# Optimization experiments

Measured on AMD Instinct MI355X. Metric: run time of the kernel, lower is better.

## Reference

```python
import jax, jax.numpy as jnp
import numpy as np

D_MODEL = 1024
FF_SIZE = 4096
H = 16
DK = D_MODEL // H
MASK_VAL = -1e15
EPS = 1e-5


def setup_inputs() -> dict:
    key = jax.random.key(0)
    ks = jax.random.split(key, 16)
    B, M, d = 2, 2048, D_MODEL
    s = 1.0 / np.sqrt(d)
    inp = {
        "x": jax.random.normal(ks[0], (B, M, d), dtype=jnp.float32),
        "mask": jnp.ones((B, M), dtype=bool),
        "Wq": jax.random.normal(ks[1], (d, d), dtype=jnp.float32) * s,
        "bq": jnp.zeros((d,), jnp.float32),
        "Wk": jax.random.normal(ks[2], (d, d), dtype=jnp.float32) * s,
        "bk": jnp.zeros((d,), jnp.float32),
        "Wv": jax.random.normal(ks[3], (d, d), dtype=jnp.float32) * s,
        "bv": jnp.zeros((d,), jnp.float32),
        "W1": jax.random.normal(ks[4], (d, FF_SIZE), dtype=jnp.float32) * s,
        "b1": jnp.zeros((FF_SIZE,), jnp.float32),
        "W2": jax.random.normal(ks[5], (FF_SIZE, d), dtype=jnp.float32) / np.sqrt(FF_SIZE),
        "b2": jnp.zeros((d,), jnp.float32),
        "g1": jnp.ones((d,), jnp.float32),
        "beta1": jnp.zeros((d,), jnp.float32),
        "g2": jnp.ones((d,), jnp.float32),
        "beta2": jnp.zeros((d,), jnp.float32),
    }
    return inp


def _layernorm(x, g, b):
    mu = jnp.mean(x, axis=-1, keepdims=True)
    var = jnp.var(x, axis=-1, keepdims=True)
    return (x - mu) * jax.lax.rsqrt(var + EPS) * g + b


def _forward(x, mask, Wq, bq, Wk, bk, Wv, bv, W1, b1, W2, b2, g1, beta1, g2, beta2):
    B, M, d = x.shape
    q = (x @ Wq + bq).reshape(B, M, H, DK)
    k = (x @ Wk + bk).reshape(B, M, H, DK)
    v = (x @ Wv + bv).reshape(B, M, H, DK)
    # att: [B, H, Mq, Mk]
    att = jnp.einsum("bqhd,bkhd->bhqk", q, k)
    if mask is not None:
        m = (mask[:, None, :] & mask[:, :, None])[:, None, :, :]  # [B,1,Mq,Mk]
        att = jnp.where(m, att, MASK_VAL)
    # NOTE: original divides by d_model (not sqrt(dk))
    att = jax.nn.softmax(att / D_MODEL, axis=-1)
    attn_out = jnp.einsum("bhqk,bkhd->bqhd", att, v).reshape(B, M, d)
    h1 = _layernorm(x + attn_out, g1, beta1)
    ff = jax.nn.relu(h1 @ W1 + b1) @ W2 + b2
    return _layernorm(h1 + ff, g2, beta2)


def reference(x, mask, Wq, bq, Wk, bk, Wv, bv, W1, b1, W2, b2, g1, beta1, g2, beta2):
    return _forward(x, mask, Wq, bq, Wk, bk, Wv, bv, W1, b1, W2, b2, g1, beta1, g2, beta2)
```

## Files before the change

### kernel.cpp

```cpp
#include <hip/hip_runtime.h>
#include <hip/hip_bf16.h>


typedef __bf16 bf16;
typedef __attribute__((ext_vector_type(8))) __bf16 bf16x8;
typedef __attribute__((ext_vector_type(4))) __bf16 bf16x4;
typedef __attribute__((ext_vector_type(4))) float f32x4;

#define MFMA16(a, b, c) __builtin_amdgcn_mfma_f32_16x16x32_bf16(a, b, c, 0, 0, 0)

__device__ __forceinline__ void ld_g2l16(void* lds, const void* g) {
  __builtin_amdgcn_global_load_lds((const __attribute__((address_space(1))) void*)g,
                                   (__attribute__((address_space(3))) void*)lds,
                                   16, 0, 0);
}

__global__ __launch_bounds__(256) void detect_dtype(const void* __restrict__ x,
                                                    int* __restrict__ flag) {
  const unsigned short* u = (const unsigned short*)x;
  int cnt = 0;
  for (int i = threadIdx.x; i < 4096; i += 256) {
    const int e = (u[i] >> 7) & 0xFF;
    if (e >= 140) ++cnt;
  }
  __shared__ int sh[256];
  sh[threadIdx.x] = cnt;
  __syncthreads();
  for (int s = 128; s > 0; s >>= 1) {
    if (threadIdx.x < s) sh[threadIdx.x] += sh[threadIdx.x + s];
    __syncthreads();
  }
  if (threadIdx.x == 0) *flag = (sh[0] > 100) ? 1 : 0;
}

__device__ __forceinline__ bf16 load_any(const void* p, size_t i, int fl) {
  return fl ? (bf16)((const float*)p)[i] : ((const bf16*)p)[i];
}

__global__ __launch_bounds__(256) void convert_x(const void* __restrict__ in,
                                                 bf16* __restrict__ o,
                                                 const int* __restrict__ flag) {
  const int fl = *flag;
  const size_t i0 = (size_t)(blockIdx.x * 256 + threadIdx.x) * 4;
#pragma unroll
  for (int i = 0; i < 4; ++i) o[i0 + i] = load_any(in, i0 + i, fl);
}

__global__ __launch_bounds__(256) void convert_small(
    const void* p0, const void* p1, const void* p2, const void* p3,
    const void* p4, const void* p5, const void* p6, const void* p7,
    const void* p8, bf16* __restrict__ dst, const int* __restrict__ flag) {
  const int fl = *flag;
  const int t = blockIdx.x * 256 + threadIdx.x;
  const void* ps[9] = {p0, p1, p2, p3, p4, p5, p6, p7, p8};
  const int sz[9]  = {1024, 1024, 1024, 4096, 1024, 1024, 1024, 1024, 1024};
  const int off[9] = {0, 1024, 2048, 3072, 7168, 8192, 9216, 10240, 11264};
#pragma unroll
  for (int a = 0; a < 9; ++a)
    if (t < sz[a]) dst[off[a] + t] = load_any(ps[a], t, fl);
}

__global__ __launch_bounds__(256) void transpose_w(const void* __restrict__ in,
                                                   bf16* __restrict__ out,
                                                   int R, int C,
                                                   const int* __restrict__ flag) {
  const int fl = *flag;
  __shared__ bf16 t[32][33];
  const int r0 = blockIdx.y * 32, c0 = blockIdx.x * 32;
  const int tx = threadIdx.x, ty = threadIdx.y;
#pragma unroll
  for (int i = ty; i < 32; i += 8)
    t[i][tx] = load_any(in, (size_t)(r0 + i) * C + c0 + tx, fl);
  __syncthreads();
#pragma unroll
  for (int i = ty; i < 32; i += 8)
    out[(size_t)(c0 + i) * R + r0 + tx] = t[tx][i];
}

__global__ __launch_bounds__(256) void transpose_w3(const void* __restrict__ q,
                                                    const void* __restrict__ k,
                                                    const void* __restrict__ v,
                                                    bf16* __restrict__ out,
                                                    const int* __restrict__ flag) {
  const int fl = *flag;
  const int z = blockIdx.z;
  const void* in = (z == 0) ? q : (z == 1) ? k : v;
  bf16* o = out + (size_t)z * 1024 * 1024;
  __shared__ bf16 t[32][33];
  const int r0 = blockIdx.y * 32, c0 = blockIdx.x * 32;
  const int tx = threadIdx.x, ty = threadIdx.y;
#pragma unroll
  for (int i = ty; i < 32; i += 8)
    t[i][tx] = load_any(in, (size_t)(r0 + i) * 1024 + c0 + tx, fl);
  __syncthreads();
#pragma unroll
  for (int i = ty; i < 32; i += 8)
    o[(size_t)(c0 + i) * 1024 + r0 + tx] = t[tx][i];
}

__global__ __launch_bounds__(256) void transpose_v(const bf16* __restrict__ qkvb,
                                                   bf16* __restrict__ vT) {
  __shared__ bf16 t[32][33];
  const int bh = blockIdx.z;
  const int b = bh >> 4, h = bh & 15;
  const int m0 = blockIdx.x * 32, d0 = blockIdx.y * 32;
  const int tx = threadIdx.x, ty = threadIdx.y;
#pragma unroll
  for (int i = ty; i < 32; i += 8)
    t[i][tx] = qkvb[(size_t)(b * 2048 + m0 + i) * 3072 + 2048 + h * 64 + d0 + tx];
  __syncthreads();
#pragma unroll
  for (int i = ty; i < 32; i += 8)
    vT[((size_t)bh * 64 + d0 + i) * 2048 + m0 + tx] = t[tx][i];
}

__global__ __launch_bounds__(256) void gemm_bt(const bf16* __restrict__ A,
                                               const bf16* __restrict__ BT,
                                               const bf16* __restrict__ bias,
                                               bf16* __restrict__ C,
                                               int M, int N, int K, int relu) {
  __shared__ bf16 sA[2][128 * 32];
  __shared__ bf16 sB[2][128 * 32];
  const int tid = threadIdx.x;
  const int wave = tid >> 6, lane = tid & 63;
  const int wm = wave >> 1, wn = wave & 1;
  const int gx = N >> 7;
  const int L = blockIdx.x;
  const int x8 = L & 7;
  const int t1 = L >> 3;
  const int cb = t1 % gx;
  const int rb = (t1 / gx) * 8 + x8;
  const int bm = rb * 128, bn = cb * 128;
  const int m16 = lane & 15, kg = lane >> 4;
  const int srow = lane >> 2;
  const int sswz = ((lane & 3) ^ ((srow >> 1) & 3)) * 8;
  const int kswz = (kg ^ ((m16 >> 1) & 3)) * 8;

  f32x4 acc[4][4];
#pragma unroll
  for (int i = 0; i < 4; ++i)
#pragma unroll
    for (int j = 0; j < 4; ++j) acc[i][j] = (f32x4){0.f, 0.f, 0.f, 0.f};

  for (int k0 = 0; k0 < K; k0 += 64) {
#pragma unroll
    for (int i = 0; i < 2; ++i) {
      const int c = wave * 2 + i;
      const int row = c * 16 + srow;
#pragma unroll
      for (int h = 0; h < 2; ++h) {
        ld_g2l16(&sA[h][c * 512], A + (size_t)(bm + row) * K + k0 + h * 32 + sswz);
        ld_g2l16(&sB[h][c * 512], BT + (size_t)(bn + row) * K + k0 + h * 32 + sswz);
      }
    }
    __syncthreads();

#pragma unroll
    for (int ks = 0; ks < 2; ++ks) {
      bf16x8 af[4], bfr[4];
#pragma unroll
      for (int t = 0; t < 4; ++t) {
        af[t]  = *(const bf16x8*)&sA[ks][(wm * 64 + t * 16 + m16) * 32 + kswz];
        bfr[t] = *(const bf16x8*)&sB[ks][(wn * 64 + t * 16 + m16) * 32 + kswz];
      }
#pragma unroll
      for (int mt = 0; mt < 4; ++mt)
#pragma unroll
        for (int nt = 0; nt < 4; ++nt)
          acc[mt][nt] = MFMA16(af[mt], bfr[nt], acc[mt][nt]);
    }
    __syncthreads();
  }

  const int r0 = bm + wm * 64, c0 = bn + wn * 64;
#pragma unroll
  for (int nt = 0; nt < 4; ++nt) {
    const int col = c0 + nt * 16 + m16;
    const float bv = (float)bias[col];
#pragma unroll
    for (int mt = 0; mt < 4; ++mt) {
#pragma unroll
      for (int r = 0; r < 4; ++r) {
        const int row = r0 + mt * 16 + kg * 4 + r;
        float v = acc[mt][nt][r] + bv;
        if (relu) v = fmaxf(v, 0.f);
        C[(size_t)row * N + col] = (bf16)v;
      }
    }
  }
}

__global__ __launch_bounds__(256) void gemm_bt64_sk(const bf16* __restrict__ A,
                                                    const bf16* __restrict__ BT,
                                                    bf16* __restrict__ C0,
                                                    bf16* __restrict__ C1,
                                                    int M, int N, int Kf, int Kp) {
  __shared__ bf16 sA[2][128 * 32];
  __shared__ bf16 sB[2][64 * 32];
  const int tid = threadIdx.x;
  const int wave = tid >> 6, lane = tid & 63;
  const int L = blockIdx.x;
  const int x8 = L & 7;
  const int t1 = L >> 3;
  const int cb = t1 & 15;
  const int u = t1 >> 4;
  const int z = u & 1;
  const int rb = (u >> 1) * 8 + x8;
  const int bm = rb * 128, bn = cb * 64;
  const int kbase = z * Kp;
  const int m16 = lane & 15, kg = lane >> 4;
  const int srow = lane >> 2;
  const int sswz = ((lane & 3) ^ ((srow >> 1) & 3)) * 8;
  const int kswz = (kg ^ ((m16 >> 1) & 3)) * 8;

  f32x4 acc[2][4];
#pragma unroll
  for (int i = 0; i < 2; ++i)
#pragma unroll
    for (int j = 0; j < 4; ++j) acc[i][j] = (f32x4){0.f, 0.f, 0.f, 0.f};

  for (int k0 = 0; k0 < Kp; k0 += 64) {
#pragma unroll
    for (int i = 0; i < 2; ++i) {
      const int c = wave * 2 + i;
      const int row = bm + c * 16 + srow;
#pragma unroll
      for (int h = 0; h < 2; ++h)
        ld_g2l16(&sA[h][c * 512], A + (size_t)row * Kf + kbase + k0 + h * 32 + sswz);
    }
    {
      const int row = bn + wave * 16 + srow;
#pragma unroll
      for (int h = 0; h < 2; ++h)
        ld_g2l16(&sB[h][wave * 512], BT + (size_t)row * Kf + kbase + k0 + h * 32 + sswz);
    }
    __syncthreads();

#pragma unroll
    for (int ks = 0; ks < 2; ++ks) {
      bf16x8 af[2], bfr[4];
#pragma unroll
      for (int t = 0; t < 2; ++t)
        af[t] = *(const bf16x8*)&sA[ks][(wave * 32 + t * 16 + m16) * 32 + kswz];
#pragma unroll
      for (int t = 0; t < 4; ++t)
        bfr[t] = *(const bf16x8*)&sB[ks][(t * 16 + m16) * 32 + kswz];
#pragma unroll
      for (int mt = 0; mt < 2; ++mt)
#pragma unroll
        for (int nt = 0; nt < 4; ++nt)
          acc[mt][nt] = MFMA16(af[mt], bfr[nt], acc[mt][nt]);
    }
    __syncthreads();
  }

  bf16* C = z ? C1 : C0;
  const int r0 = bm + wave * 32;
#pragma unroll
  for (int nt = 0; nt < 4; ++nt) {
    const int col = bn + nt * 16 + m16;
#pragma unroll
    for (int mt = 0; mt < 2; ++mt) {
#pragma unroll
      for (int r = 0; r < 4; ++r) {
        const int row = r0 + mt * 16 + kg * 4 + r;
        C[(size_t)row * N + col] = (bf16)acc[mt][nt][r];
      }
    }
  }
}

__global__ __launch_bounds__(256) void attn_kernel(const bf16* __restrict__ qkvb,
                                                   const bf16* __restrict__ vT,
                                                   bf16* __restrict__ op0,
                                                   bf16* __restrict__ op1,
                                                   float* __restrict__ den0,
                                                   float* __restrict__ den1) {
  __shared__ bf16 sK[2][64 * 32];
  __shared__ bf16 sV[2][64 * 32];
  __shared__ bf16 pl[4][2][16 * 72];
  const int L = blockIdx.x;
  const int x8 = L & 7;
  const int t1 = L >> 3;
  const int qt = t1 & 15;
  const int c  = (t1 >> 4) * 8 + x8;
  const int h  = c & 15;
  const int z  = c >> 4;
  const int b = z >> 1, kh = z & 1;
  const int tid = threadIdx.x, wv = tid >> 6, lane = tid & 63;
  const int m16 = lane & 15, kg = lane >> 4;
  const int srow = lane >> 2;
  const int sswz = ((lane & 3) ^ ((srow >> 1) & 3)) * 8;
  const int kswz = (kg ^ ((m16 >> 1) & 3)) * 8;

  const float qs = 1.4426950408889634f / 1024.0f;
  bf16x8 fq0[2], fq1[2];
#pragma unroll
  for (int f = 0; f < 2; ++f) {
    const int q0 = qt * 128 + f * 64 + wv * 16;
    const bf16* qp = qkvb + (size_t)(b * 2048 + q0 + m16) * 3072 + h * 64;
    bf16x8 a = *(const bf16x8*)(qp + kg * 8);
    bf16x8 cc = *(const bf16x8*)(qp + 32 + kg * 8);
#pragma unroll
    for (int i = 0; i < 8; ++i) {
      a[i] = (bf16)((float)a[i] * qs);
      cc[i] = (bf16)((float)cc[i] * qs);
    }
    fq0[f] = a;
    fq1[f] = cc;
  }

  bf16x8 ones;
#pragma unroll
  for (int i = 0; i < 8; ++i) ones[i] = (bf16)1.0f;

  f32x4 o[2][4], oden[2];
#pragma unroll
  for (int f = 0; f < 2; ++f) {
#pragma unroll
    for (int cl = 0; cl < 4; ++cl) o[f][cl] = (f32x4){0.f, 0.f, 0.f, 0.f};
    oden[f] = (f32x4){0.f, 0.f, 0.f, 0.f};
  }

  const bf16* kbase = qkvb + (size_t)(b * 2048) * 3072 + 1024 + h * 64;
  const bf16* vbase = vT + (size_t)(b * 16 + h) * 64 * 2048;
  bf16* plw0 = &pl[wv][0][0];
  bf16* plw1 = &pl[wv][1][0];

  const int tstart = kh * 1024;
  for (int t0 = tstart; t0 < tstart + 1024; t0 += 64) {
    {
      const int row = wv * 16 + srow;
      ld_g2l16(&sK[0][wv * 512], kbase + (size_t)(t0 + row) * 3072 + sswz);
      ld_g2l16(&sK[1][wv * 512], kbase + (size_t)(t0 + row) * 3072 + 32 + sswz);
      ld_g2l16(&sV[0][wv * 512], vbase + (size_t)row * 2048 + t0 + sswz);
      ld_g2l16(&sV[1][wv * 512], vbase + (size_t)row * 2048 + t0 + 32 + sswz);
    }
    __syncthreads();

    __builtin_amdgcn_s_setprio(1);
#pragma unroll
    for (int g = 0; g < 4; ++g) {
      const bf16x8 af0 = *(const bf16x8*)&sK[0][(g * 16 + m16) * 32 + kswz];
      const bf16x8 af1 = *(const bf16x8*)&sK[1][(g * 16 + m16) * 32 + kswz];
#pragma unroll
      for (int f = 0; f < 2; ++f) {
        f32x4 zz = (f32x4){0.f, 0.f, 0.f, 0.f};
        zz = MFMA16(af0, fq0[f], zz);
        zz = MFMA16(af1, fq1[f], zz);
        bf16x4 pv4;
#pragma unroll
        for (int r = 0; r < 4; ++r)
          pv4[r] = (bf16)__builtin_amdgcn_exp2f(zz[r]);
        *(bf16x4*)((f ? plw1 : plw0) + m16 * 72 + g * 16 + kg * 4) = pv4;
      }
    }
    __builtin_amdgcn_s_setprio(0);
    __asm__ __volatile__("s_waitcnt lgkmcnt(0)" ::: "memory");

    __builtin_amdgcn_s_setprio(1);
#pragma unroll
    for (int tt = 0; tt < 2; ++tt) {
      const bf16x8 pa0 = *(const bf16x8*)(plw0 + m16 * 72 + tt * 32 + kg * 8);
      const bf16x8 pa1 = *(const bf16x8*)(plw1 + m16 * 72 + tt * 32 + kg * 8);
      oden[0] = MFMA16(pa0, ones, oden[0]);
      oden[1] = MFMA16(pa1, ones, oden[1]);
#pragma unroll
      for (int cl = 0; cl < 4; ++cl) {
        const bf16x8 fv = *(const bf16x8*)&sV[tt][(cl * 16 + m16) * 32 + kswz];
        o[0][cl] = MFMA16(pa0, fv, o[0][cl]);
        o[1][cl] = MFMA16(pa1, fv, o[1][cl]);
      }
    }
    __builtin_amdgcn_s_setprio(0);
    __syncthreads();
  }

  bf16* op = kh ? op1 : op0;
  float* dptr = kh ? den1 : den0;
#pragma unroll
  for (int f = 0; f < 2; ++f)
#pragma unroll
    for (int r = 0; r < 4; ++r) {
      const int row = qt * 128 + f * 64 + wv * 16 + kg * 4 + r;
      if (m16 == 0) dptr[((b * 16 + h) << 11) + row] = oden[f][r];
      bf16* opp = op + (size_t)(b * 2048 + row) * 1024 + h * 64;
#pragma unroll
      for (int cl = 0; cl < 4; ++cl) opp[cl * 16 + m16] = (bf16)o[f][cl][r];
    }
}

__global__ __launch_bounds__(256) void ln1_kernel(const bf16* __restrict__ x,
                                                  const bf16* __restrict__ op0,
                                                  const bf16* __restrict__ op1,
                                                  const float* __restrict__ den0,
                                                  const float* __restrict__ den1,
                                                  const bf16* __restrict__ g,
                                                  const bf16* __restrict__ be,
                                                  bf16* __restrict__ h1b) {
  const int row = blockIdx.x;
  const int b = row >> 11, q = row & 2047;
  const size_t base = (size_t)row * 1024;
  const int t = threadIdx.x;
  const int h = t >> 4;
  const float rden = 1.0f / (den0[((b * 16 + h) << 11) + q] +
                             den1[((b * 16 + h) << 11) + q]);
  float v[4], s = 0.f, ss = 0.f;
#pragma unroll
  for (int i = 0; i < 4; ++i) {
    const int c = t * 4 + i;
    const float at = ((float)op0[base + c] + (float)op1[base + c]) * rden;
    const float xv = (float)x[base + c] + at;
    v[i] = xv; s += xv; ss += xv * xv;
  }
#pragma unroll
  for (int m = 1; m < 64; m <<= 1) { s += __shfl_xor(s, m); ss += __shfl_xor(ss, m); }
  __shared__ float rs[4], rss[4];
  const int wave = t >> 6, lane = t & 63;
  if (lane == 0) { rs[wave] = s; rss[wave] = ss; }
  __syncthreads();
  s = rs[0] + rs[1] + rs[2] + rs[3];
  ss = rss[0] + rss[1] + rss[2] + rss[3];
  const float mu = s * (1.f / 1024.f);
  const float var = fmaxf(ss * (1.f / 1024.f) - mu * mu, 0.f);
  const float rstd = rsqrtf(var + 1e-5f);
#pragma unroll
  for (int i = 0; i < 4; ++i) {
    const int c = t * 4 + i;
    h1b[base + c] = (bf16)((v[i] - mu) * rstd * (float)g[c] + (float)be[c]);
  }
}

__global__ __launch_bounds__(256) void ln2_kernel(const bf16* __restrict__ h1b,
                                                  const bf16* __restrict__ p0,
                                                  const bf16* __restrict__ p1,
                                                  const bf16* __restrict__ b2,
                                                  const bf16* __restrict__ g,
                                                  const bf16* __restrict__ be,
                                                  void* __restrict__ out,
                                                  const int* __restrict__ flag) {
  const int fl = *flag;
  const int row = blockIdx.x;
  const size_t base = (size_t)row * 1024;
  const int t = threadIdx.x;
  float v[4], s = 0.f, ss = 0.f;
#pragma unroll
  for (int i = 0; i < 4; ++i) {
    const int c = t * 4 + i;
    const float xv = (float)h1b[base + c] + (float)p0[base + c] +
                     (float)p1[base + c] + (float)b2[c];
    v[i] = xv; s += xv; ss += xv * xv;
  }
#pragma unroll
  for (int m = 1; m < 64; m <<= 1) { s += __shfl_xor(s, m); ss += __shfl_xor(ss, m); }
  __shared__ float rs[4], rss[4];
  const int wave = t >> 6, lane = t & 63;
  if (lane == 0) { rs[wave] = s; rss[wave] = ss; }
  __syncthreads();
  s = rs[0] + rs[1] + rs[2] + rs[3];
  ss = rss[0] + rss[1] + rss[2] + rss[3];
  const float mu = s * (1.f / 1024.f);
  const float var = fmaxf(ss * (1.f / 1024.f) - mu * mu, 0.f);
  const float rstd = rsqrtf(var + 1e-5f);
#pragma unroll
  for (int i = 0; i < 4; ++i) {
    const int c = t * 4 + i;
    const float y = (v[i] - mu) * rstd * (float)g[c] + (float)be[c];
    if (fl) ((float*)out)[base + c] = y;
    else    ((bf16*)out)[base + c] = (bf16)y;
  }
}

extern "C" void kernel_launch(void* const* d_in, const int* in_sizes, int n_in,
                              void* d_out, int out_size, void* d_ws, size_t ws_size,
                              hipStream_t stream) {
  const void* x   = d_in[0];
  const void* Wq  = d_in[2];
  const void* bq  = d_in[3];
  const void* Wk  = d_in[4];
  const void* bk  = d_in[5];
  const void* Wv  = d_in[6];
  const void* bv  = d_in[7];
  const void* W1  = d_in[8];
  const void* b1  = d_in[9];
  const void* W2  = d_in[10];
  const void* b2  = d_in[11];
  const void* g1  = d_in[12];
  const void* be1 = d_in[13];
  const void* g2  = d_in[14];
  const void* be2 = d_in[15];

  const size_t MB = 1u << 20;
  char* w = (char*)d_ws;
  int*  flag = (int*)w;
  bf16* sm   = (bf16*)(w + 65536);
  bf16* bqkvc = sm + 0;
  bf16* b1c   = sm + 3072;
  bf16* b2c   = sm + 7168;
  bf16* g1c   = sm + 8192;
  bf16* be1c  = sm + 9216;
  bf16* g2c   = sm + 10240;
  bf16* be2c  = sm + 11264;
  float* den0 = (float*)(w + 512 * 1024);
  float* den1 = (float*)(w + 768 * 1024);
  bf16* xc    = (bf16*)(w + 1 * MB);
  bf16* WqkvT = (bf16*)(w + 9 * MB);
  bf16* W1T   = (bf16*)(w + 15 * MB);
  bf16* W2T   = (bf16*)(w + 23 * MB);
  bf16* qkvb  = (bf16*)(w + 31 * MB);
  bf16* vT    = (bf16*)(w + 55 * MB);
  bf16* op0   = (bf16*)(w + 63 * MB);
  bf16* op1   = (bf16*)(w + 71 * MB);
  bf16* h1b   = (bf16*)(w + 71 * MB);
  bf16* ff1   = (bf16*)(w + 31 * MB);
  bf16* ff2p0 = (bf16*)(w + 1 * MB);
  bf16* ff2p1 = (bf16*)(w + 63 * MB);

  detect_dtype<<<1, 256, 0, stream>>>(x, flag);
  convert_x<<<4096, 256, 0, stream>>>(x, xc, flag);
  convert_small<<<16, 256, 0, stream>>>(bq, bk, bv, b1, b2, g1, be1, g2, be2,
                                        sm, flag);

  const dim3 tb(32, 8);
  transpose_w3<<<dim3(32, 32, 3), tb, 0, stream>>>(Wq, Wk, Wv, WqkvT, flag);
  transpose_w<<<dim3(128, 32), tb, 0, stream>>>(W1, W1T, 1024, 4096, flag);
  transpose_w<<<dim3(32, 128), tb, 0, stream>>>(W2, W2T, 4096, 1024, flag);

  gemm_bt<<<24 * 32, 256, 0, stream>>>(xc, WqkvT, bqkvc, qkvb,
                                       4096, 3072, 1024, 0);

  transpose_v<<<dim3(64, 2, 32), tb, 0, stream>>>(qkvb, vT);
  attn_kernel<<<1024, 256, 0, stream>>>(qkvb, vT, op0, op1, den0, den1);

  ln1_kernel<<<4096, 256, 0, stream>>>(xc, op0, op1, den0, den1,
                                       g1c, be1c, h1b);

  gemm_bt<<<32 * 32, 256, 0, stream>>>(h1b, W1T, b1c, ff1,
                                       4096, 4096, 1024, 1);
  gemm_bt64_sk<<<1024, 256, 0, stream>>>(ff1, W2T, ff2p0, ff2p1,
                                         4096, 1024, 4096, 2048);

  ln2_kernel<<<4096, 256, 0, stream>>>(h1b, ff2p0, ff2p1, b2c, g2c, be2c,
                                       d_out, flag);
}
```

Before: 354.5 us.

## Replace 128x128 GEMM with 256x256-tile, 512-thread double-buffered prefetch kernel

Replaces the QKV and FF1 projection GEMM with a new kernel. Each block computes a 256x256 output tile with 8 waves and a BK=64 LDS stage, and prefetches the tile two steps ahead. A partial vmcnt wait plus barriers let global-to-LDS loads overlap the MFMA loop, and s_setprio raises priority during the MFMA phase. The larger tile improves data reuse and cuts synchronization per FLOP. In exchange it uses 128KB of LDS per block and launches only 192 or 256 blocks, so CU occupancy and load balance may suffer.

```diff
diff --git a/kernel.cpp b/kernel.cpp
--- a/kernel.cpp
+++ b/kernel.cpp
@@ -114,75 +114,98 @@
     vT[((size_t)bh * 64 + d0 + i) * 2048 + m0 + tx] = t[tx][i];
 }
 
-__global__ __launch_bounds__(256) void gemm_bt(const bf16* __restrict__ A,
-                                               const bf16* __restrict__ BT,
-                                               const bf16* __restrict__ bias,
-                                               bf16* __restrict__ C,
-                                               int M, int N, int K, int relu) {
-  __shared__ bf16 sA[2][128 * 32];
-  __shared__ bf16 sB[2][128 * 32];
+__global__ __launch_bounds__(512, 2) void gemm_bt256(const bf16* __restrict__ A,
+                                                     const bf16* __restrict__ BT,
+                                                     const bf16* __restrict__ bias,
+                                                     bf16* __restrict__ C,
+                                                     int M, int N, int K, int relu) {
+  __shared__ bf16 sA[2][256 * 64];
+  __shared__ bf16 sB[2][256 * 64];
   const int tid = threadIdx.x;
-  const int wave = tid >> 6, lane = tid & 63;
-  const int wm = wave >> 1, wn = wave & 1;
-  const int gx = N >> 7;
+  const int w = tid >> 6, lane = tid & 63;
+  const int wm = w >> 2, wn = w & 3;
+  const int m16 = lane & 15, kg = lane >> 4;
+  const int gx = N >> 8;
   const int L = blockIdx.x;
-  const int x8 = L & 7;
-  const int t1 = L >> 3;
-  const int cb = t1 % gx;
-  const int rb = (t1 / gx) * 8 + x8;
-  const int bm = rb * 128, bn = cb * 128;
-  const int m16 = lane & 15, kg = lane >> 4;
-  const int srow = lane >> 2;
-  const int sswz = ((lane & 3) ^ ((srow >> 1) & 3)) * 8;
-  const int kswz = (kg ^ ((m16 >> 1) & 3)) * 8;
-
-  f32x4 acc[4][4];
-#pragma unroll
-  for (int i = 0; i < 4; ++i)
+  const int x8 = L & 7, t1 = L >> 3;
+  const int cb = t1 % gx, rb = (t1 / gx) * 8 + x8;
+  const int bm = rb * 256, bn = cb * 256;
+  const int strow = lane >> 3;
+  const int sslot = ((lane & 7) ^ strow) * 8;
+  const int s0 = (kg ^ (m16 & 7)) * 8;
+  const int s1 = ((kg + 4) ^ (m16 & 7)) * 8;
+
+#define STAGE256(p, k0)                                                         \
+  do {                                                                          \
+    _Pragma("unroll")                                                           \
+    for (int n_ = 0; n_ < 4; ++n_) {                                            \
+      ld_g2l16(&sA[p][n_ * 4096 + w * 512],                                     \
+               A + (size_t)(bm + n_ * 64 + w * 8 + strow) * K + (k0) + sslot);  \
+      ld_g2l16(&sB[p][n_ * 4096 + w * 512],                                     \
+               BT + (size_t)(bn + n_ * 64 + w * 8 + strow) * K + (k0) + sslot); \
+    }                                                                           \
+  } while (0)
+
+  f32x4 acc[8][4];
+#pragma unroll
+  for (int i = 0; i < 8; ++i)
 #pragma unroll
     for (int j = 0; j < 4; ++j) acc[i][j] = (f32x4){0.f, 0.f, 0.f, 0.f};
 
-  for (int k0 = 0; k0 < K; k0 += 64) {
-#pragma unroll
-    for (int i = 0; i < 2; ++i) {
-      const int c = wave * 2 + i;
-      const int row = c * 16 + srow;
-#pragma unroll
-      for (int h = 0; h < 2; ++h) {
-        ld_g2l16(&sA[h][c * 512], A + (size_t)(bm + row) * K + k0 + h * 32 + sswz);
-        ld_g2l16(&sB[h][c * 512], BT + (size_t)(bn + row) * K + k0 + h * 32 + sswz);
+  STAGE256(0, 0);
+  STAGE256(1, 64);
+
+  const int NT = K >> 6;
+  for (int t = 0; t < NT; ++t) {
+    const int p = t & 1;
+    if (t < NT - 1)
+      __asm__ __volatile__("s_waitcnt vmcnt(8)" ::: "memory");
+    else
+      __asm__ __volatile__("s_waitcnt vmcnt(0)" ::: "memory");
+    __builtin_amdgcn_s_barrier();
+
+    const bf16* pA = &sA[p][(wm * 128 + m16) * 64];
+    const bf16* pB = &sB[p][(wn * 64 + m16) * 64];
+    bf16x8 bfr[4][2];
+#pragma unroll
+    for (int nf = 0; nf < 4; ++nf) {
+      bfr[nf][0] = *(const bf16x8*)(pB + nf * 1024 + s0);
+      bfr[nf][1] = *(const bf16x8*)(pB + nf * 1024 + s1);
+    }
+    bf16x8 af[8][2];
+#pragma unroll
+    for (int mf = 0; mf < 8; ++mf) {
+      af[mf][0] = *(const bf16x8*)(pA + mf * 1024 + s0);
+      af[mf][1] = *(const bf16x8*)(pA + mf * 1024 + s1);
+    }
+    __asm__ __volatile__("s_waitcnt lgkmcnt(0)" ::: "memory");
+    __builtin_amdgcn_s_barrier();
+
+    if (t + 2 < NT) STAGE256(p, (t + 2) * 64);
+
+    __builtin_amdgcn_s_setprio(1);
+#pragma unroll
+    for (int mf = 0; mf < 8; ++mf)
+#pragma unroll
+      for (int nf = 0; nf < 4; ++nf) {
+        acc[mf][nf] = MFMA16(af[mf][0], bfr[nf][0], acc[mf][nf]);
+        acc[mf][nf] = MFMA16(af[mf][1], bfr[nf][1], acc[mf][nf]);
       }
-    }
-    __syncthreads();
-
-#pragma unroll
-    for (int ks = 0; ks < 2; ++ks) {
-      bf16x8 af[4], bfr[4];
-#pragma unroll
-      for (int t = 0; t < 4; ++t) {
-        af[t]  = *(const bf16x8*)&sA[ks][(wm * 64 + t * 16 + m16) * 32 + kswz];
-        bfr[t] = *(const bf16x8*)&sB[ks][(wn * 64 + t * 16 + m16) * 32 + kswz];
-      }
-#pragma unroll
-      for (int mt = 0; mt < 4; ++mt)
-#pragma unroll
-        for (int nt = 0; nt < 4; ++nt)
-          acc[mt][nt] = MFMA16(af[mt], bfr[nt], acc[mt][nt]);
-    }
-    __syncthreads();
-  }
-
-  const int r0 = bm + wm * 64, c0 = bn + wn * 64;
-#pragma unroll
-  for (int nt = 0; nt < 4; ++nt) {
-    const int col = c0 + nt * 16 + m16;
+    __builtin_amdgcn_s_setprio(0);
+  }
+#undef STAGE256
+
+  const int r0 = bm + wm * 128, c0 = bn + wn * 64;
+#pragma unroll
+  for (int nf = 0; nf < 4; ++nf) {
+    const int col = c0 + nf * 16 + m16;
     const float bv = (float)bias[col];
 #pragma unroll
-    for (int mt = 0; mt < 4; ++mt) {
+    for (int mf = 0; mf < 8; ++mf) {
 #pragma unroll
       for (int r = 0; r < 4; ++r) {
-        const int row = r0 + mt * 16 + kg * 4 + r;
-        float v = acc[mt][nt][r] + bv;
+        const int row = r0 + mf * 16 + kg * 4 + r;
+        float v = acc[mf][nf][r] + bv;
         if (relu) v = fmaxf(v, 0.f);
         C[(size_t)row * N + col] = (bf16)v;
       }
@@ -526,8 +549,8 @@
   transpose_w<<<dim3(128, 32), tb, 0, stream>>>(W1, W1T, 1024, 4096, flag);
   transpose_w<<<dim3(32, 128), tb, 0, stream>>>(W2, W2T, 4096, 1024, flag);
 
-  gemm_bt<<<24 * 32, 256, 0, stream>>>(xc, WqkvT, bqkvc, qkvb,
-                                       4096, 3072, 1024, 0);
+  gemm_bt256<<<16 * 12, 512, 0, stream>>>(xc, WqkvT, bqkvc, qkvb,
+                                          4096, 3072, 1024, 0);
 
   transpose_v<<<dim3(64, 2, 32), tb, 0, stream>>>(qkvb, vT);
   attn_kernel<<<1024, 256, 0, stream>>>(qkvb, vT, op0, op1, den0, den1);
@@ -535,8 +558,8 @@
   ln1_kernel<<<4096, 256, 0, stream>>>(xc, op0, op1, den0, den1,
                                        g1c, be1c, h1b);
 
-  gemm_bt<<<32 * 32, 256, 0, stream>>>(h1b, W1T, b1c, ff1,
-                                       4096, 4096, 1024, 1);
+  gemm_bt256<<<16 * 16, 512, 0, stream>>>(h1b, W1T, b1c, ff1,
+                                          4096, 4096, 1024, 1);
   gemm_bt64_sk<<<1024, 256, 0, stream>>>(ff1, W2T, ff2p0, ff2p1,
                                          4096, 1024, 4096, 2048);
 
```

Measured after the change: 343.1 us. 3.2% less time.
